# Kernel tuning notes

Measured on AMD Instinct MI355X. Metric: run time of the kernel, lower is better.

## Reference

```python
import jax, jax.numpy as jnp
import numpy as np

NUM_CLASSES = 1000
NUM_NEIGHBOURS = 200
SIGMA = 10.0
GAUSS_CONST = 1.0 / (2.0 * SIGMA ** 2)


def setup_inputs() -> dict:
    key = jax.random.key(0)
    k1, k2, k3 = jax.random.split(key, 3)
    B, D, C = 512, 512, 100000
    features = jax.random.normal(k1, (B, D), dtype=jnp.float32)
    centres = jax.random.normal(k2, (C, D), dtype=jnp.float32)
    centre_labels = jax.random.randint(k3, (C,), 0, NUM_CLASSES)
    weight = jnp.zeros((C,), dtype=jnp.float32)
    return {"features": features, "centres": centres,
            "centre_labels": centre_labels, "weight": weight}


def _knn(features, centres, k):
    # squared euclidean distances [B, C] without materializing [B, C, D]
    f2 = jnp.sum(features * features, axis=1, keepdims=True)      # [B,1]
    c2 = jnp.sum(centres * centres, axis=1)                        # [C]
    d2 = f2 + c2[None, :] - 2.0 * features @ centres.T             # [B,C]
    _, idx = jax.lax.top_k(-d2, k)                                 # smallest k
    return idx                                                     # [B,k]


def reference(features, centres, centre_labels, weight):
    B = features.shape[0]
    K = NUM_NEIGHBOURS
    nbr = _knn(features, centres, K)                               # [B,K] int
    gathered = centres[nbr]                                        # [B,K,D]
    d2 = jnp.sum((features[:, None, :] - gathered) ** 2, axis=-1)  # [B,K]
    kernel_weights = jnp.exp(weight)                               # [C]
    d = jnp.exp(-d2 * GAUSS_CONST) * kernel_weights[nbr]           # [B,K]
    nbr_labels = centre_labels[nbr]                                # [B,K]
    rows = jnp.arange(B)[:, None]
    p = jnp.zeros((B, NUM_CLASSES), dtype=d.dtype).at[rows, nbr_labels].add(d)
    p = jnp.where(p == 0, 1e-10, p)
    p = p / jnp.sum(p, axis=1, keepdims=True)
    return jnp.log(p)
```

## Files before the change

### kernel.cpp

```cpp
#include <hip/hip_runtime.h>
#include <hip/hip_fp16.h>
#include <math.h>
#include <stdint.h>

#define D_DIM    512
#define NCLS     1000
#define KSEL     200
#define NBINS    1024
#define CAND_MAX 2048
#define GCONST   0.005
#define MARGIN   2.0f

typedef short s8v __attribute__((ext_vector_type(8)));
typedef float f4v __attribute__((ext_vector_type(4)));

#define GLOAD_LDS16(gp, lp) __builtin_amdgcn_global_load_lds( \
    (const __attribute__((address_space(1))) void*)(gp),      \
    (__attribute__((address_space(3))) void*)(lp), 16, 0, 0)

static __device__ __forceinline__ unsigned short f2bf(float x) {
    unsigned u = __float_as_uint(x);
    return (unsigned short)((u + 0x7FFFu + ((u >> 16) & 1u)) >> 16);
}

__global__ __launch_bounds__(256)
void convertF(const float* __restrict__ F, unsigned short* __restrict__ Fb,
              float* __restrict__ f2)
{
    __shared__ float red[256];
    const int r = blockIdx.x, t = threadIdx.x;
    float2 v = *(const float2*)(F + (size_t)r * D_DIM + t * 2);
    ushort2 o; o.x = f2bf(v.x); o.y = f2bf(v.y);
    *(ushort2*)(Fb + (size_t)r * D_DIM + t * 2) = o;
    red[t] = v.x * v.x + v.y * v.y;
    __syncthreads();
    for (int off = 128; off > 0; off >>= 1) {
        if (t < off) red[t] += red[t + off];
        __syncthreads();
    }
    if (t == 0) f2[r] = red[0];
}

__global__ __launch_bounds__(256)
void convertC(const float* __restrict__ C, unsigned short* __restrict__ Cb,
              float* __restrict__ c2, int N)
{
    const int lane   = threadIdx.x & 63;
    const int wglob  = (int)((blockIdx.x * 256 + threadIdx.x) >> 6);
    const int nwaves = (int)((gridDim.x * 256) >> 6);
    for (int row = wglob; row < N; row += nwaves) {
        const float* rp = C + (size_t)row * D_DIM;
        float4 a = *(const float4*)(rp + lane * 8);
        float4 b = *(const float4*)(rp + lane * 8 + 4);
        float s = a.x*a.x + a.y*a.y + a.z*a.z + a.w*a.w
                + b.x*b.x + b.y*b.y + b.z*b.z + b.w*b.w;
        uint4 o;
        o.x = (unsigned)f2bf(a.x) | ((unsigned)f2bf(a.y) << 16);
        o.y = (unsigned)f2bf(a.z) | ((unsigned)f2bf(a.w) << 16);
        o.z = (unsigned)f2bf(b.x) | ((unsigned)f2bf(b.y) << 16);
        o.w = (unsigned)f2bf(b.z) | ((unsigned)f2bf(b.w) << 16);
        *(uint4*)(Cb + (size_t)row * D_DIM + lane * 8) = o;
#pragma unroll
        for (int off = 32; off > 0; off >>= 1) s += __shfl_down(s, off, 64);
        if (lane == 0) c2[row] = s;
    }
}

__global__ __launch_bounds__(256)
void mfma_gemm(const unsigned short* __restrict__ Fb,
               const unsigned short* __restrict__ Cb,
               __half* __restrict__ Sm, int N)
{
    __shared__ short smem[2 * 128 * 64];
    short* As = smem;
    short* Bs = smem + 128 * 64;
    const int t    = threadIdx.x;
    const int lane = t & 63;
    const int w    = t >> 6;
    const int wm   = w >> 1, wn = w & 1;
    const int m0   = blockIdx.y * 128;
    const int n0   = blockIdx.x * 128;
    const int lrow = lane >> 3;
    const int koct = ((lane & 7) ^ (lrow & 7)) * 8;

    f4v acc[4][4];
#pragma unroll
    for (int i = 0; i < 4; ++i)
#pragma unroll
        for (int j = 0; j < 4; ++j) acc[i][j] = (f4v){0.f, 0.f, 0.f, 0.f};

    const int quad = lane >> 4;
    const int col  = lane & 15;

    for (int k0 = 0; k0 < D_DIM; k0 += 64) {
#pragma unroll
        for (int cc = 0; cc < 4; ++cc) {
            int ch = w * 4 + cc;
            const unsigned short* ga =
                Fb + (size_t)(m0 + ch * 8 + lrow) * D_DIM + k0 + koct;
            GLOAD_LDS16(ga, &As[ch * 512]);
            const unsigned short* gb =
                Cb + (size_t)(n0 + ch * 8 + lrow) * D_DIM + k0 + koct;
            GLOAD_LDS16(gb, &Bs[ch * 512]);
        }
        __syncthreads();
#pragma unroll
        for (int kk = 0; kk < 2; ++kk) {
            s8v a[4], b[4];
#pragma unroll
            for (int i = 0; i < 4; ++i) {
                int row = wm * 64 + i * 16 + col;
                int slot = (kk * 4 + quad) ^ (col & 7);
                a[i] = *(s8v*)&As[row * 64 + slot * 8];
            }
#pragma unroll
            for (int j = 0; j < 4; ++j) {
                int row = wn * 64 + j * 16 + col;
                int slot = (kk * 4 + quad) ^ (col & 7);
                b[j] = *(s8v*)&Bs[row * 64 + slot * 8];
            }
#pragma unroll
            for (int i = 0; i < 4; ++i)
#pragma unroll
                for (int j = 0; j < 4; ++j)
                    acc[i][j] = __builtin_amdgcn_mfma_f32_16x16x32_bf16(
                        a[i], b[j], acc[i][j], 0, 0, 0);
        }
        __syncthreads();
    }

    __half* Cs = (__half*)smem;
#pragma unroll
    for (int i = 0; i < 4; ++i) {
#pragma unroll
        for (int j = 0; j < 4; ++j) {
#pragma unroll
            for (int v = 0; v < 4; ++v) {
                int ml = wm * 64 + i * 16 + quad * 4 + v;
                int nl = wn * 64 + j * 16 + col;
                int slot = ((nl >> 3) ^ (ml & 7));
                Cs[ml * 128 + slot * 8 + (nl & 7)] = __float2half(acc[i][j][v]);
            }
        }
    }
    __syncthreads();
#pragma unroll
    for (int it = 0; it < 8; ++it) {
        int idx = it * 256 + t;
        int row = idx >> 4;
        int oct = idx & 15;
        int n   = n0 + oct * 8;
        const __half* src = &Cs[row * 128 + ((oct ^ (row & 7)) * 8)];
        __half* dst = Sm + (size_t)(m0 + row) * N + n;
        if (n + 7 < N) {
            *(uint4*)dst = *(const uint4*)src;
        } else if (n < N) {
            for (int e = 0; e < 8 && n + e < N; ++e) dst[e] = src[e];
        }
    }
}

__global__ __launch_bounds__(1024)
void fused_select(const __half* __restrict__ Sm, const float* __restrict__ f2,
                  const float* __restrict__ c2,
                  const float* __restrict__ F, const float* __restrict__ C,
                  const int* __restrict__ labels, const float* __restrict__ weight,
                  float* __restrict__ out, int N)
{
    __shared__ unsigned hist[NBINS];
    __shared__ float    fs[D_DIM];
    __shared__ int      idxs[CAND_MAX];
    __shared__ double   dists[CAND_MAX];
    __shared__ float    p[NCLS];
    __shared__ float    red[1024];
    __shared__ unsigned scanbuf[256];
    __shared__ float    sT;
    __shared__ unsigned scnt;

    const int r = blockIdx.x, t = threadIdx.x;
    for (int b = t; b < NBINS; b += 1024) hist[b] = 0u;
    for (int c = t; c < NCLS; c += 1024) p[c] = 0.f;
    for (int k = t; k < D_DIM; k += 1024) fs[k] = F[(size_t)r * D_DIM + k];
    if (t == 0) { sT = 1e30f; scnt = 0u; }
    __syncthreads();

    const float fr = f2[r];
    const __half* srow = Sm + (size_t)r * N;

    for (int j = t * 8; j < N; j += 8192) {
        uint4 sv = *(const uint4*)(srow + j);
        float4 ca = *(const float4*)(c2 + j);
        float4 cb = *(const float4*)(c2 + j + 4);
        float2 s0 = __half22float2(*(__half2*)&sv.x);
        float2 s1 = __half22float2(*(__half2*)&sv.y);
        float2 s2 = __half22float2(*(__half2*)&sv.z);
        float2 s3 = __half22float2(*(__half2*)&sv.w);
        float d2v[8] = { fr + ca.x - 2.f * s0.x, fr + ca.y - 2.f * s0.y,
                         fr + ca.z - 2.f * s1.x, fr + ca.w - 2.f * s1.y,
                         fr + cb.x - 2.f * s2.x, fr + cb.y - 2.f * s2.y,
                         fr + cb.z - 2.f * s3.x, fr + cb.w - 2.f * s3.y };
#pragma unroll
        for (int e = 0; e < 8; ++e) {
            int b = (int)(d2v[e] * 0.5f);
            b = b < 0 ? 0 : (b > NBINS - 1 ? NBINS - 1 : b);
            atomicAdd(&hist[b], 1u);
        }
    }
    __syncthreads();

    if (t < 256) {
        unsigned loc[NBINS / 256];
        unsigned s = 0;
#pragma unroll
        for (int i = 0; i < NBINS / 256; ++i) {
            loc[i] = hist[t * (NBINS / 256) + i];
            s += loc[i];
        }
        scanbuf[t] = s;
        __syncthreads();
        unsigned pre = 0;
        for (int u = 0; u < t; ++u) pre += scanbuf[u];
        if (pre < KSEL && pre + s >= KSEL) {
            unsigned cum = pre;
            int b = NBINS - 1;
#pragma unroll
            for (int i = 0; i < NBINS / 256; ++i) {
                cum += loc[i];
                if (cum >= KSEL) { b = t * (NBINS / 256) + i; break; }
            }
            sT = 2.0f * (float)(b + 1) + MARGIN;
        }
    } else {
        __syncthreads();
    }
    __syncthreads();
    const float Tr = sT;

    for (int j = t * 8; j < N; j += 8192) {
        uint4 sv = *(const uint4*)(srow + j);
        float4 ca = *(const float4*)(c2 + j);
        float4 cb = *(const float4*)(c2 + j + 4);
        float2 s0 = __half22float2(*(__half2*)&sv.x);
        float2 s1 = __half22float2(*(__half2*)&sv.y);
        float2 s2 = __half22float2(*(__half2*)&sv.z);
        float2 s3 = __half22float2(*(__half2*)&sv.w);
        float d2v[8] = { fr + ca.x - 2.f * s0.x, fr + ca.y - 2.f * s0.y,
                         fr + ca.z - 2.f * s1.x, fr + ca.w - 2.f * s1.y,
                         fr + cb.x - 2.f * s2.x, fr + cb.y - 2.f * s2.y,
                         fr + cb.z - 2.f * s3.x, fr + cb.w - 2.f * s3.y };
#pragma unroll
        for (int e = 0; e < 8; ++e) {
            if (d2v[e] <= Tr) {
                unsigned pos = atomicAdd(&scnt, 1u);
                if (pos < CAND_MAX) idxs[pos] = j + e;
            }
        }
    }
    __syncthreads();
    int Nc = (int)scnt;
    if (Nc > CAND_MAX) Nc = CAND_MAX;

    {
        const int wv = t >> 6, lane = t & 63;
        for (int i = wv; i < Nc; i += 16) {
            int ci = idxs[i];
            const float* cp = C + (size_t)ci * D_DIM;
            float4 a  = *(const float4*)(cp + lane * 8);
            float4 b  = *(const float4*)(cp + lane * 8 + 4);
            float4 fa = *(const float4*)(fs + lane * 8);
            float4 fb = *(const float4*)(fs + lane * 8 + 4);
            double d0 = (double)fa.x - (double)a.x;
            double d1 = (double)fa.y - (double)a.y;
            double d2 = (double)fa.z - (double)a.z;
            double d3 = (double)fa.w - (double)a.w;
            double d4 = (double)fb.x - (double)b.x;
            double d5 = (double)fb.y - (double)b.y;
            double d6 = (double)fb.z - (double)b.z;
            double d7 = (double)fb.w - (double)b.w;
            double acc = d0*d0 + d1*d1 + d2*d2 + d3*d3
                       + d4*d4 + d5*d5 + d6*d6 + d7*d7;
#pragma unroll
            for (int off = 32; off > 0; off >>= 1)
                acc += __shfl_down(acc, off, 64);
            if (lane == 0) dists[i] = acc;
        }
    }
    __syncthreads();

    int ksel = KSEL < Nc ? KSEL : Nc;
    for (int i = t; i < Nc; i += 1024) {
        double di = dists[i];
        int    ii = idxs[i];
        int rank = 0;
        for (int j = 0; j < Nc; ++j) {
            double dj = dists[j];
            rank += (dj < di) || (dj == di && idxs[j] < ii);
        }
        if (rank < ksel) {
            double wgt = exp(-di * GCONST) * exp((double)weight[ii]);
            atomicAdd(&p[labels[ii]], (float)wgt);
        }
    }
    __syncthreads();

    float s = 0.f;
    for (int c = t; c < NCLS; c += 1024) {
        float v = p[c];
        if (v == 0.f) v = 1e-10f;
        p[c] = v;
        s += v;
    }
    red[t] = s;
    __syncthreads();
    for (int o = 512; o > 0; o >>= 1) {
        if (t < o) red[t] += red[t + o];
        __syncthreads();
    }
    float total = red[0];
    for (int c = t; c < NCLS; c += 1024)
        out[(size_t)r * NCLS + c] = logf(p[c] / total);
}

extern "C" void kernel_launch(void* const* d_in, const int* in_sizes, int n_in,
                              void* d_out, int out_size, void* d_ws, size_t ws_size,
                              hipStream_t stream)
{
    const float* features = (const float*)d_in[0];
    const float* centres  = (const float*)d_in[1];
    const int*   labels   = (const int*)d_in[2];
    const float* weight   = (const float*)d_in[3];
    const int B = in_sizes[0] / D_DIM;
    const int N = in_sizes[2];
    float* out = (float*)d_out;

    uint8_t* w = (uint8_t*)d_ws;
    size_t off = 0;
    auto alloc = [&](size_t bytes) -> uint8_t* {
        uint8_t* ptr = w + off;
        off = (off + bytes + 255) & ~(size_t)255;
        return ptr;
    };
    float*          f2 = (float*)alloc((size_t)B * 4);
    float*          c2 = (float*)alloc((size_t)N * 4);
    unsigned short* Fb = (unsigned short*)alloc((size_t)B * D_DIM * 2);
    unsigned short* Cb = (unsigned short*)alloc((size_t)N * D_DIM * 2);
    __half*         Sm = (__half*)alloc((size_t)B * N * 2);
    (void)ws_size;

    convertF<<<B, 256, 0, stream>>>(features, Fb, f2);
    convertC<<<1024, 256, 0, stream>>>(centres, Cb, c2, N);

    dim3 ggrid((N + 127) / 128, B / 128);
    mfma_gemm<<<ggrid, 256, 0, stream>>>(Fb, Cb, Sm, N);

    fused_select<<<B, 1024, 0, stream>>>(Sm, f2, c2, features, centres,
                                         labels, weight, out, N);
}
```

Baseline: 491.3 us.

## Fuse centre bf16 conversion and norm computation into GEMM B-tile load

Removes the separate convertC pass and the bf16 copy of centres. The GEMM now reads fp32 centres directly, converts them to bf16 in registers, writes them to LDS, and accumulates the squared norms. Only the m0==0 blocks write the norms out. The grid is transposed so the four M-blocks that share a centre tile run next to each other, which gives L2 reuse of the fp32 reads. The next k-slice is register-prefetched to hide load latency. The trade-off is that each centre tile is read four times as fp32 (twice the bytes of bf16) and converted redundantly, in exchange for dropping a full write/read of the bf16 copy and one kernel launch.

```diff
diff --git a/kernel.cpp b/kernel.cpp
--- a/kernel.cpp
+++ b/kernel.cpp
@@ -42,33 +42,9 @@
 }
 
 __global__ __launch_bounds__(256)
-void convertC(const float* __restrict__ C, unsigned short* __restrict__ Cb,
-              float* __restrict__ c2, int N)
-{
-    const int lane   = threadIdx.x & 63;
-    const int wglob  = (int)((blockIdx.x * 256 + threadIdx.x) >> 6);
-    const int nwaves = (int)((gridDim.x * 256) >> 6);
-    for (int row = wglob; row < N; row += nwaves) {
-        const float* rp = C + (size_t)row * D_DIM;
-        float4 a = *(const float4*)(rp + lane * 8);
-        float4 b = *(const float4*)(rp + lane * 8 + 4);
-        float s = a.x*a.x + a.y*a.y + a.z*a.z + a.w*a.w
-                + b.x*b.x + b.y*b.y + b.z*b.z + b.w*b.w;
-        uint4 o;
-        o.x = (unsigned)f2bf(a.x) | ((unsigned)f2bf(a.y) << 16);
-        o.y = (unsigned)f2bf(a.z) | ((unsigned)f2bf(a.w) << 16);
-        o.z = (unsigned)f2bf(b.x) | ((unsigned)f2bf(b.y) << 16);
-        o.w = (unsigned)f2bf(b.z) | ((unsigned)f2bf(b.w) << 16);
-        *(uint4*)(Cb + (size_t)row * D_DIM + lane * 8) = o;
-#pragma unroll
-        for (int off = 32; off > 0; off >>= 1) s += __shfl_down(s, off, 64);
-        if (lane == 0) c2[row] = s;
-    }
-}
-
-__global__ __launch_bounds__(256)
 void mfma_gemm(const unsigned short* __restrict__ Fb,
-               const unsigned short* __restrict__ Cb,
+               const float* __restrict__ C,
+               float* __restrict__ c2g,
                __half* __restrict__ Sm, int N)
 {
     __shared__ short smem[2 * 128 * 64];
@@ -78,44 +54,77 @@
     const int lane = t & 63;
     const int w    = t >> 6;
     const int wm   = w >> 1, wn = w & 1;
-    const int m0   = blockIdx.y * 128;
-    const int n0   = blockIdx.x * 128;
+    const int m0   = blockIdx.x * 128;
+    const int n0   = blockIdx.y * 128;
     const int lrow = lane >> 3;
-    const int koct = ((lane & 7) ^ (lrow & 7)) * 8;
-
-    f4v acc[4][4];
-#pragma unroll
-    for (int i = 0; i < 4; ++i)
-#pragma unroll
-        for (int j = 0; j < 4; ++j) acc[i][j] = (f4v){0.f, 0.f, 0.f, 0.f};
-
+    const int oct  = (lane & 7) ^ lrow;
     const int quad = lane >> 4;
     const int col  = lane & 15;
 
+    f4v acc[4][4];
+#pragma unroll
+    for (int i = 0; i < 4; ++i)
+#pragma unroll
+        for (int j = 0; j < 4; ++j) acc[i][j] = (f4v){0.f, 0.f, 0.f, 0.f};
+
+    float  c2part[4] = {0.f, 0.f, 0.f, 0.f};
+    float4 ra[4], rb[4];
+
+#pragma unroll
+    for (int cc = 0; cc < 4; ++cc) {
+        int row = (w * 4 + cc) * 8 + lrow;
+        int rg  = n0 + row; rg = rg < N ? rg : N - 1;
+        const float* gp = C + (size_t)rg * D_DIM + oct * 8;
+        ra[cc] = *(const float4*)gp;
+        rb[cc] = *(const float4*)(gp + 4);
+    }
+
     for (int k0 = 0; k0 < D_DIM; k0 += 64) {
+        __syncthreads();
 #pragma unroll
         for (int cc = 0; cc < 4; ++cc) {
             int ch = w * 4 + cc;
-            const unsigned short* ga =
-                Fb + (size_t)(m0 + ch * 8 + lrow) * D_DIM + k0 + koct;
-            GLOAD_LDS16(ga, &As[ch * 512]);
-            const unsigned short* gb =
-                Cb + (size_t)(n0 + ch * 8 + lrow) * D_DIM + k0 + koct;
-            GLOAD_LDS16(gb, &Bs[ch * 512]);
-        }
-        __syncthreads();
+            GLOAD_LDS16(Fb + (size_t)(m0 + ch * 8 + lrow) * D_DIM + k0 + oct * 8,
+                        &As[ch * 512]);
+        }
+#pragma unroll
+        for (int cc = 0; cc < 4; ++cc) {
+            int row = (w * 4 + cc) * 8 + lrow;
+            float4 va = ra[cc], vb = rb[cc];
+            c2part[cc] += va.x*va.x + va.y*va.y + va.z*va.z + va.w*va.w
+                        + vb.x*vb.x + vb.y*vb.y + vb.z*vb.z + vb.w*vb.w;
+            uint4 o;
+            o.x = (unsigned)f2bf(va.x) | ((unsigned)f2bf(va.y) << 16);
+            o.y = (unsigned)f2bf(va.z) | ((unsigned)f2bf(va.w) << 16);
+            o.z = (unsigned)f2bf(vb.x) | ((unsigned)f2bf(vb.y) << 16);
+            o.w = (unsigned)f2bf(vb.z) | ((unsigned)f2bf(vb.w) << 16);
+            *(uint4*)&Bs[row * 64 + (lane & 7) * 8] = o;
+        }
+        __syncthreads();
+
+        if (k0 + 64 < D_DIM) {
+#pragma unroll
+            for (int cc = 0; cc < 4; ++cc) {
+                int row = (w * 4 + cc) * 8 + lrow;
+                int rg  = n0 + row; rg = rg < N ? rg : N - 1;
+                const float* gp = C + (size_t)rg * D_DIM + (k0 + 64) + oct * 8;
+                ra[cc] = *(const float4*)gp;
+                rb[cc] = *(const float4*)(gp + 4);
+            }
+        }
+
 #pragma unroll
         for (int kk = 0; kk < 2; ++kk) {
             s8v a[4], b[4];
 #pragma unroll
             for (int i = 0; i < 4; ++i) {
-                int row = wm * 64 + i * 16 + col;
+                int row  = wm * 64 + i * 16 + col;
                 int slot = (kk * 4 + quad) ^ (col & 7);
                 a[i] = *(s8v*)&As[row * 64 + slot * 8];
             }
 #pragma unroll
             for (int j = 0; j < 4; ++j) {
-                int row = wn * 64 + j * 16 + col;
+                int row  = wn * 64 + j * 16 + col;
                 int slot = (kk * 4 + quad) ^ (col & 7);
                 b[j] = *(s8v*)&Bs[row * 64 + slot * 8];
             }
@@ -126,9 +135,20 @@
                     acc[i][j] = __builtin_amdgcn_mfma_f32_16x16x32_bf16(
                         a[i], b[j], acc[i][j], 0, 0, 0);
         }
-        __syncthreads();
-    }
-
+    }
+
+#pragma unroll
+    for (int cc = 0; cc < 4; ++cc) {
+        float s = c2part[cc];
+        s += __shfl_xor(s, 1, 64);
+        s += __shfl_xor(s, 2, 64);
+        s += __shfl_xor(s, 4, 64);
+        int row = (w * 4 + cc) * 8 + lrow;
+        if (m0 == 0 && (lane & 7) == 0 && (n0 + row) < N)
+            c2g[n0 + row] = s;
+    }
+
+    __syncthreads();
     __half* Cs = (__half*)smem;
 #pragma unroll
     for (int i = 0; i < 4; ++i) {
@@ -148,9 +168,9 @@
     for (int it = 0; it < 8; ++it) {
         int idx = it * 256 + t;
         int row = idx >> 4;
-        int oct = idx & 15;
-        int n   = n0 + oct * 8;
-        const __half* src = &Cs[row * 128 + ((oct ^ (row & 7)) * 8)];
+        int o8  = idx & 15;
+        int n   = n0 + o8 * 8;
+        const __half* src = &Cs[row * 128 + ((o8 ^ (row & 7)) * 8)];
         __half* dst = Sm + (size_t)(m0 + row) * N + n;
         if (n + 7 < N) {
             *(uint4*)dst = *(const uint4*)src;
@@ -343,15 +363,13 @@
     float*          f2 = (float*)alloc((size_t)B * 4);
     float*          c2 = (float*)alloc((size_t)N * 4);
     unsigned short* Fb = (unsigned short*)alloc((size_t)B * D_DIM * 2);
-    unsigned short* Cb = (unsigned short*)alloc((size_t)N * D_DIM * 2);
     __half*         Sm = (__half*)alloc((size_t)B * N * 2);
     (void)ws_size;
 
     convertF<<<B, 256, 0, stream>>>(features, Fb, f2);
-    convertC<<<1024, 256, 0, stream>>>(centres, Cb, c2, N);
-
-    dim3 ggrid((N + 127) / 128, B / 128);
-    mfma_gemm<<<ggrid, 256, 0, stream>>>(Fb, Cb, Sm, N);
+
+    dim3 ggrid(B / 128, (N + 127) / 128);
+    mfma_gemm<<<ggrid, 256, 0, stream>>>(Fb, centres, c2, Sm, N);
 
     fused_select<<<B, 1024, 0, stream>>>(Sm, f2, c2, features, centres,
                                          labels, weight, out, N);
```

After: 488.8 us. About the same (-0.5%).
